# Kernel tuning notes

Hardware: AMD Instinct MI355X
Metric: run time of the kernel (lower is better)

The kernel has to match this reference:

```python
import jax, jax.numpy as jnp
import numpy as np


def setup_inputs() -> dict:
    key = jax.random.key(0)
    k1, _ = jax.random.split(key)
    x = jax.random.normal(k1, (8, 128, 56, 56), dtype=jnp.float32)
    gamma = jnp.array(0.5, dtype=jnp.float32)  # learned scalar (init gamma=0.5)
    return {"x": x, "gamma": gamma}


def reference(x, gamma):
    # conv=False path: query/key/value convs are Identity, so Q=K=V=x flattened.
    B, C, H, W = x.shape
    N = H * W
    v = x.reshape(B, C, N)                          # [B, C, N]
    # energy[b, i, j] = sum_c x[b, c, i] * x[b, c, j]  (Q^T K)
    energy = jnp.einsum('bci,bcj->bij', v, v)       # [B, N, N]
    # multiplicative mask: zero out the diagonal BEFORE softmax (not -inf)
    mask = 1.0 - jnp.eye(N, dtype=energy.dtype)
    attention = jax.nn.softmax(energy * mask, axis=-1)  # [B, N, N]
    # out = bmm(V, attention): out[b, c, j] = sum_i v[b, c, i] * attention[b, i, j]
    out = jnp.einsum('bci,bij->bcj', v, attention)  # [B, C, N]
    out = jax.nn.relu(out).reshape(B, C, H, W)
    y = gamma * out + x
    return (y, out, x, gamma)
```

## Files before the change

kernel.cpp:

```cpp
#include <hip/hip_runtime.h>
#include <math.h>

#define Bb 8
#define Cc 128
#define Nn 3136
#define Np 3200
#define Mm (Bb*Cc*Nn)
#define PADX 136
#define PADV 72
#define SHIFT 44.0f

typedef unsigned short u16;
typedef unsigned int   u32;
typedef __attribute__((ext_vector_type(8)))  u16      u16x8;
typedef __attribute__((ext_vector_type(8)))  _Float16 f16x8;
typedef __attribute__((ext_vector_type(4)))  _Float16 f16x4;
typedef __attribute__((ext_vector_type(4)))  float    f32x4;
typedef __attribute__((ext_vector_type(16))) float    f32x16;

__global__ __launch_bounds__(256) void prep_kernel(const float* __restrict__ x,
                                                   const float* __restrict__ gamma_p,
                                                   float* __restrict__ out,
                                                   u16* __restrict__ xt,
                                                   u16* __restrict__ xc,
                                                   float* __restrict__ row_d) {
    const int bx = blockIdx.x;
    const int b = bx / 50, nblk = bx % 50;
    const int t = threadIdx.x;

    if (nblk == 49) {
        const u16x8 z8 = {0, 0, 0, 0, 0, 0, 0, 0};
        #pragma unroll
        for (int it = 0; it < 4; ++it) {
            const int idx = it * 256 + t, row = idx / 17, seg = idx % 17;
            *(u16x8*)&xt[(size_t)(b * Np + Nn + row) * PADX + seg * 8] = z8;
        }
        if (t < 64) {
            const int idx = 1024 + t, row = idx / 17, seg = idx % 17;
            *(u16x8*)&xt[(size_t)(b * Np + Nn + row) * PADX + seg * 8] = z8;
        }
        #pragma unroll
        for (int it = 0; it < 4; ++it) {
            const int idx = it * 256 + t, c = idx >> 3, seg = idx & 7;
            *(u16x8*)&xc[(size_t)(b * Cc + c) * Np + Nn + seg * 8] = z8;
        }
        if (t < 64) row_d[b * Np + Nn + t] = 1.0f;
        return;
    }

    __shared__ float lx[Cc][65];
    const int n0 = nblk * 64;

    #pragma unroll 8
    for (int r = 0; r < 32; ++r) {
        const int c = r * 4 + (t >> 6);
        const int g = (b * Cc + c) * Nn + n0 + (t & 63);
        const float v = x[g];
        lx[c][t & 63] = v;
        out[(size_t)2 * Mm + g] = v;
    }
    __syncthreads();

    {
        const int nl = t & 63, cseg = t >> 6;
        u16x8 hv[4];
        #pragma unroll
        for (int cc = 0; cc < 32; ++cc) {
            const _Float16 hh = (_Float16)lx[cseg * 32 + cc][nl];
            hv[cc >> 3][cc & 7] = __builtin_bit_cast(u16, hh);
        }
        const size_t base = (size_t)(b * Np + n0 + nl) * PADX + cseg * 32;
        #pragma unroll
        for (int k = 0; k < 4; ++k) *(u16x8*)&xt[base + k * 8] = hv[k];
    }
    {
        const int c = t >> 1, half = t & 1;
        u16x8 hv[4];
        #pragma unroll
        for (int k = 0; k < 32; ++k) {
            const _Float16 hh = (_Float16)lx[c][half * 32 + k];
            hv[k >> 3][k & 7] = __builtin_bit_cast(u16, hh);
        }
        const size_t base = (size_t)(b * Cc + c) * Np + n0 + half * 32;
        #pragma unroll
        for (int k = 0; k < 4; ++k) *(u16x8*)&xc[base + k * 8] = hv[k];
    }
    if (bx == 0 && t == 0) out[(size_t)3 * Mm] = gamma_p[0];
}

__global__ __launch_bounds__(256, 3) void stats_kernel(const u16* __restrict__ xt,
                                                       float* __restrict__ row_d) {
    __shared__ u16 s_jt[64 * PADX];

    const int bx = blockIdx.x;
    const int b = bx / 196, rem = bx % 196;
    const int i0 = (rem >> 2) * 64, jq = rem & 3;
    const int t = threadIdx.x;
    const int w = t >> 6, l = t & 63, lane = l & 31, h = l >> 5;
    const int igrp = w & 1, jsub = w >> 1;

    f16x8 Bf[8];
    {
        const size_t rb = (size_t)(b * Np + i0 + igrp * 32 + lane) * PADX + h * 8;
        #pragma unroll
        for (int kk = 0; kk < 8; ++kk)
            Bf[kk] = *(const f16x8*)&xt[rb + kk * 16];
    }

    float sa = 0.0f, sb = 0.0f;
    const int jt0 = jq * 12 + (jq < 2 ? jq : 2);
    const int jcnt = 12 + (jq < 2 ? 1 : 0);

    for (int jt = jt0; jt < jt0 + jcnt; ++jt) {
        const int j0 = jt * 64;
        __syncthreads();
        {
            const u16* src = xt + (size_t)(b * Np + j0) * PADX;
            u16x8 tv[4], tv4;
            #pragma unroll
            for (int it = 0; it < 4; ++it)
                tv[it] = *(const u16x8*)&src[(it * 256 + t) * 8];
            if (t < 64) tv4 = *(const u16x8*)&src[(1024 + t) * 8];
            #pragma unroll
            for (int it = 0; it < 4; ++it)
                *(u16x8*)&s_jt[(it * 256 + t) * 8] = tv[it];
            if (t < 64) *(u16x8*)&s_jt[(1024 + t) * 8] = tv4;
        }
        __syncthreads();

        f32x16 ea, eb;
        #pragma unroll
        for (int r = 0; r < 16; ++r) { ea[r] = 0.0f; eb[r] = 0.0f; }
        const int arow = (jsub * 32 + lane) * PADX + h * 8;
        #pragma unroll
        for (int kk = 0; kk < 4; ++kk) {
            const f16x8 A0 = *(const f16x8*)&s_jt[arow + (2 * kk) * 16];
            const f16x8 A1 = *(const f16x8*)&s_jt[arow + (2 * kk + 1) * 16];
            ea = __builtin_amdgcn_mfma_f32_32x32x16_f16(A0, Bf[2 * kk], ea, 0, 0, 0);
            eb = __builtin_amdgcn_mfma_f32_32x32x16_f16(A1, Bf[2 * kk + 1], eb, 0, 0, 0);
        }

        const bool diag = (j0 == i0) && (jsub == igrp);
        #pragma unroll
        for (int r = 0; r < 16; ++r) {
            const int mrow = (r & 3) + 8 * (r >> 2) + 4 * h;
            float v = ea[r] + eb[r];
            if (diag && (mrow == lane)) v = 0.0f;
            if (r & 1) sb += __expf(v - SHIFT); else sa += __expf(v - SHIFT);
        }
    }

    float ssum = sa + sb;
    ssum += __shfl_xor(ssum, 32, 64);
    if (h == 0) atomicAdd(&row_d[b * Np + i0 + igrp * 32 + lane], ssum);
}

__global__ __launch_bounds__(256, 3) void out_kernel(const u16* __restrict__ xt,
                                                     const u16* __restrict__ xc,
                                                     const float* __restrict__ row_d,
                                                     float* __restrict__ out) {
    __shared__ u16 s_xt[64 * PADX];
    __shared__ u16 s_xc[Cc * PADV];
    __shared__ u16 s_pt[64 * PADV];

    const int bx = blockIdx.x;
    const int b = bx / 98, rem = bx % 98;
    const int j0 = (rem >> 1) * 64, ih = rem & 1;
    const int t = threadIdx.x;
    const int w = t >> 6, l = t & 63, lane = l & 31, h = l >> 5;
    const int isub = w & 1, jgrp = w >> 1;
    const int jg = w & 1,  cp = w >> 1;
    const u16* __restrict__ xtb = xt + (size_t)b * Np * PADX;
    const u16* __restrict__ xcb = xc + (size_t)b * Cc * Np;

    f16x8 Bj[8];
    {
        const size_t rb = (size_t)(j0 + jgrp * 32 + lane) * PADX + h * 8;
        #pragma unroll
        for (int kk = 0; kk < 8; ++kk)
            Bj[kk] = *(const f16x8*)&xtb[rb + kk * 16];
    }

    f32x16 oa, ob;
    #pragma unroll
    for (int r = 0; r < 16; ++r) { oa[r] = 0.0f; ob[r] = 0.0f; }

    for (int ti = ih * 25; ti < ih * 25 + 25; ++ti) {
        const int i0g = ti * 64;
        __syncthreads();
        {
            const u16* srct = xtb + (size_t)i0g * PADX;
            u16x8 vt[4], vt4, vcr[4];
            #pragma unroll
            for (int it = 0; it < 4; ++it) {
                vt[it] = *(const u16x8*)&srct[(it * 256 + t) * 8];
                const int q = it * 256 + t;
                vcr[it] = *(const u16x8*)&xcb[(size_t)(q >> 3) * Np + i0g + (q & 7) * 8];
            }
            if (t < 64) vt4 = *(const u16x8*)&srct[(1024 + t) * 8];
            #pragma unroll
            for (int it = 0; it < 4; ++it) {
                *(u16x8*)&s_xt[(it * 256 + t) * 8] = vt[it];
                const int q = it * 256 + t;
                *(u16x8*)&s_xc[(q >> 3) * PADV + (q & 7) * 8] = vcr[it];
            }
            if (t < 64) *(u16x8*)&s_xt[(1024 + t) * 8] = vt4;
        }
        __syncthreads();

        f32x16 ea, eb;
        #pragma unroll
        for (int r = 0; r < 16; ++r) { ea[r] = 0.0f; eb[r] = 0.0f; }
        const int arow = (isub * 32 + lane) * PADX + h * 8;
        #pragma unroll
        for (int kk = 0; kk < 4; ++kk) {
            const f16x8 A0 = *(const f16x8*)&s_xt[arow + (2 * kk) * 16];
            const f16x8 A1 = *(const f16x8*)&s_xt[arow + (2 * kk + 1) * 16];
            ea = __builtin_amdgcn_mfma_f32_32x32x16_f16(A0, Bj[2 * kk], ea, 0, 0, 0);
            eb = __builtin_amdgcn_mfma_f32_32x32x16_f16(A1, Bj[2 * kk + 1], eb, 0, 0, 0);
        }

        const bool mayDiag = (j0 < i0g + 64) && (i0g < j0 + 64);
        const int ptbase = (jgrp * 32 + lane) * PADV + isub * 32;
        #pragma unroll
        for (int q = 0; q < 4; ++q) {
            const f32x4 dq = *(const f32x4*)&row_d[b * Np + i0g + isub * 32 + q * 8 + h * 4];
            f16x4 pv;
            #pragma unroll
            for (int r = 0; r < 4; ++r) {
                const int m = q * 8 + h * 4 + r;
                float v = ea[q * 4 + r] + eb[q * 4 + r];
                if (mayDiag && (i0g + isub * 32 + m == j0 + jgrp * 32 + lane)) v = 0.0f;
                pv[r] = (_Float16)(__expf(v - SHIFT) * __builtin_amdgcn_rcpf(dq[r]));
            }
            *(f16x4*)&s_pt[ptbase + q * 8 + h * 4] = pv;
        }
        __syncthreads();

        const int pbrow = (jg * 32 + lane) * PADV + h * 8;
        const int va0 = (cp * 64 + lane) * PADV + h * 8;
        const int va1 = va0 + 32 * PADV;
        #pragma unroll
        for (int kk = 0; kk < 4; ++kk) {
            const f16x8 Bp  = *(const f16x8*)&s_pt[pbrow + kk * 16];
            const f16x8 Av0 = *(const f16x8*)&s_xc[va0 + kk * 16];
            const f16x8 Av1 = *(const f16x8*)&s_xc[va1 + kk * 16];
            oa = __builtin_amdgcn_mfma_f32_32x32x16_f16(Av0, Bp, oa, 0, 0, 0);
            ob = __builtin_amdgcn_mfma_f32_32x32x16_f16(Av1, Bp, ob, 0, 0, 0);
        }
    }

    #pragma unroll
    for (int r = 0; r < 16; ++r) {
        const int mrow = (r & 3) + 8 * (r >> 2) + 4 * h;
        const int jj = j0 + jg * 32 + lane;
        {
            const int c = cp * 64 + mrow;
            const size_t pos = (size_t)(b * Cc + c) * Nn + jj;
            out[(size_t)ih * Mm + pos] = oa[r];
        }
        {
            const int c = cp * 64 + 32 + mrow;
            const size_t pos = (size_t)(b * Cc + c) * Nn + jj;
            out[(size_t)ih * Mm + pos] = ob[r];
        }
    }
}

__global__ __launch_bounds__(256) void finish_kernel(const float* __restrict__ x,
                                                     const float* __restrict__ gamma_p,
                                                     float* __restrict__ out) {
    const float gamma = gamma_p[0];
    const size_t base = ((size_t)blockIdx.x * 256 + threadIdx.x) * 4;
    const f32x4 pa = *(const f32x4*)&out[base];
    const f32x4 pb = *(const f32x4*)&out[(size_t)Mm + base];
    const f32x4 xv = *(const f32x4*)&x[base];
    f32x4 yo, oo;
    #pragma unroll
    for (int r = 0; r < 4; ++r) {
        const float o = fmaxf(pa[r] + pb[r], 0.0f);
        oo[r] = o;
        yo[r] = fmaf(gamma, o, xv[r]);
    }
    *(f32x4*)&out[base] = yo;
    *(f32x4*)&out[(size_t)Mm + base] = oo;
}

extern "C" void kernel_launch(void* const* d_in, const int* in_sizes, int n_in,
                              void* d_out, int out_size, void* d_ws, size_t ws_size,
                              hipStream_t stream) {
    const float* x       = (const float*)d_in[0];
    const float* gamma_p = (const float*)d_in[1];
    float* out = (float*)d_out;

    float* row_d = (float*)d_ws;
    u16* xt = (u16*)((char*)d_ws + (1 << 17));
    u16* xc = xt + (size_t)Bb * Np * PADX;

    hipMemsetAsync(row_d, 0, (size_t)Bb * Np * sizeof(float), stream);
    prep_kernel  <<<400, 256, 0, stream>>>(x, gamma_p, out, xt, xc, row_d);
    stats_kernel <<<1568, 256, 0, stream>>>(xt, row_d);
    out_kernel   <<<784, 256, 0, stream>>>(xt, xc, row_d, out);
    finish_kernel<<<3136, 256, 0, stream>>>(x, gamma_p, out);
}
```

Before: 215.2 us.

## Store fp16 operands in MFMA-fragment tiled layout and read directly from global

Changes the fp16 copies of x into a tiled layout that matches the MFMA fragment layout, so stats and out kernels load A/V operands straight from global memory (L2) instead of staging through LDS with barriers. The P tile is double-buffered in shared memory, leaving one barrier per iteration. Softmax normalization is folded into a per-row log2 offset computed by a new small conv kernel, which replaces exp and reciprocal with a single exp2 of an fma. Diagonal masking gets a separate branch, stats occupancy is raised, and block index ordering interleaves batches. This adds a kernel launch and relies on L2/L1 serving repeated global loads efficiently.

```diff
diff --git a/kernel.cpp b/kernel.cpp
--- a/kernel.cpp
+++ b/kernel.cpp
@@ -5,24 +5,35 @@
 #define Cc 128
 #define Nn 3136
 #define Np 3200
+#define NT 50
 #define Mm (Bb*Cc*Nn)
-#define PADX 136
 #define PADV 72
-#define SHIFT 44.0f
+#define L2E 1.44269504088896340736f
+#define C44 (44.0f * L2E)
+
+#define XT2B (NT*16*64*8)
+#define XC2B (NT*8*128*8)
 
 typedef unsigned short u16;
-typedef unsigned int   u32;
 typedef __attribute__((ext_vector_type(8)))  u16      u16x8;
 typedef __attribute__((ext_vector_type(8)))  _Float16 f16x8;
 typedef __attribute__((ext_vector_type(4)))  _Float16 f16x4;
 typedef __attribute__((ext_vector_type(4)))  float    f32x4;
 typedef __attribute__((ext_vector_type(16))) float    f32x16;
 
+__device__ __forceinline__ float exp2fast(float x) {
+#if __has_builtin(__builtin_amdgcn_exp2f)
+    return __builtin_amdgcn_exp2f(x);
+#else
+    float r; asm volatile("v_exp_f32 %0, %1" : "=v"(r) : "v"(x)); return r;
+#endif
+}
+
 __global__ __launch_bounds__(256) void prep_kernel(const float* __restrict__ x,
                                                    const float* __restrict__ gamma_p,
                                                    float* __restrict__ out,
-                                                   u16* __restrict__ xt,
-                                                   u16* __restrict__ xc,
+                                                   u16* __restrict__ xt2,
+                                                   u16* __restrict__ xc2,
                                                    float* __restrict__ row_d) {
     const int bx = blockIdx.x;
     const int b = bx / 50, nblk = bx % 50;
@@ -30,19 +41,12 @@
 
     if (nblk == 49) {
         const u16x8 z8 = {0, 0, 0, 0, 0, 0, 0, 0};
+        u16* dt = xt2 + ((size_t)b * NT + 49) * (16 * 64 * 8);
+        u16* dc = xc2 + ((size_t)b * NT + 49) * (8 * 128 * 8);
         #pragma unroll
         for (int it = 0; it < 4; ++it) {
-            const int idx = it * 256 + t, row = idx / 17, seg = idx % 17;
-            *(u16x8*)&xt[(size_t)(b * Np + Nn + row) * PADX + seg * 8] = z8;
-        }
-        if (t < 64) {
-            const int idx = 1024 + t, row = idx / 17, seg = idx % 17;
-            *(u16x8*)&xt[(size_t)(b * Np + Nn + row) * PADX + seg * 8] = z8;
-        }
-        #pragma unroll
-        for (int it = 0; it < 4; ++it) {
-            const int idx = it * 256 + t, c = idx >> 3, seg = idx & 7;
-            *(u16x8*)&xc[(size_t)(b * Cc + c) * Np + Nn + seg * 8] = z8;
+            *(u16x8*)&dt[(it * 256 + t) * 8] = z8;
+            *(u16x8*)&dc[(it * 256 + t) * 8] = z8;
         }
         if (t < 64) row_d[b * Np + Nn + t] = 1.0f;
         return;
@@ -69,9 +73,9 @@
             const _Float16 hh = (_Float16)lx[cseg * 32 + cc][nl];
             hv[cc >> 3][cc & 7] = __builtin_bit_cast(u16, hh);
         }
-        const size_t base = (size_t)(b * Np + n0 + nl) * PADX + cseg * 32;
-        #pragma unroll
-        for (int k = 0; k < 4; ++k) *(u16x8*)&xt[base + k * 8] = hv[k];
+        u16* base = xt2 + (((size_t)(b * NT + nblk) * 16 + cseg * 4) * 64 + nl) * 8;
+        #pragma unroll
+        for (int k = 0; k < 4; ++k) *(u16x8*)&base[k * (64 * 8)] = hv[k];
     }
     {
         const int c = t >> 1, half = t & 1;
@@ -81,170 +85,149 @@
             const _Float16 hh = (_Float16)lx[c][half * 32 + k];
             hv[k >> 3][k & 7] = __builtin_bit_cast(u16, hh);
         }
-        const size_t base = (size_t)(b * Cc + c) * Np + n0 + half * 32;
-        #pragma unroll
-        for (int k = 0; k < 4; ++k) *(u16x8*)&xc[base + k * 8] = hv[k];
+        u16* base = xc2 + (((size_t)(b * NT + nblk) * 8 + half * 4) * 128 + c) * 8;
+        #pragma unroll
+        for (int k = 0; k < 4; ++k) *(u16x8*)&base[k * (128 * 8)] = hv[k];
     }
     if (bx == 0 && t == 0) out[(size_t)3 * Mm] = gamma_p[0];
 }
 
-__global__ __launch_bounds__(256, 3) void stats_kernel(const u16* __restrict__ xt,
+__global__ __launch_bounds__(256, 5) void stats_kernel(const u16* __restrict__ xt2,
                                                        float* __restrict__ row_d) {
-    __shared__ u16 s_jt[64 * PADX];
-
     const int bx = blockIdx.x;
-    const int b = bx / 196, rem = bx % 196;
-    const int i0 = (rem >> 2) * 64, jq = rem & 3;
+    const int b = bx & 7, rem = bx >> 3;
+    const int i0t = rem >> 2, jq = rem & 3;
     const int t = threadIdx.x;
     const int w = t >> 6, l = t & 63, lane = l & 31, h = l >> 5;
     const int igrp = w & 1, jsub = w >> 1;
+    const u16* __restrict__ xb = xt2 + (size_t)b * XT2B;
 
     f16x8 Bf[8];
-    {
-        const size_t rb = (size_t)(b * Np + i0 + igrp * 32 + lane) * PADX + h * 8;
-        #pragma unroll
-        for (int kk = 0; kk < 8; ++kk)
-            Bf[kk] = *(const f16x8*)&xt[rb + kk * 16];
-    }
-
-    float sa = 0.0f, sb = 0.0f;
+    const int irow = igrp * 32 + lane;
+    #pragma unroll
+    for (int kk = 0; kk < 8; ++kk)
+        Bf[kk] = *(const f16x8*)&xb[(((size_t)i0t * 16 + 2 * kk + h) * 64 + irow) * 8];
+
+    float sa = 0.f, sb = 0.f;
     const int jt0 = jq * 12 + (jq < 2 ? jq : 2);
     const int jcnt = 12 + (jq < 2 ? 1 : 0);
+    const int jrow = jsub * 32 + lane;
 
     for (int jt = jt0; jt < jt0 + jcnt; ++jt) {
-        const int j0 = jt * 64;
-        __syncthreads();
-        {
-            const u16* src = xt + (size_t)(b * Np + j0) * PADX;
-            u16x8 tv[4], tv4;
-            #pragma unroll
-            for (int it = 0; it < 4; ++it)
-                tv[it] = *(const u16x8*)&src[(it * 256 + t) * 8];
-            if (t < 64) tv4 = *(const u16x8*)&src[(1024 + t) * 8];
-            #pragma unroll
-            for (int it = 0; it < 4; ++it)
-                *(u16x8*)&s_jt[(it * 256 + t) * 8] = tv[it];
-            if (t < 64) *(u16x8*)&s_jt[(1024 + t) * 8] = tv4;
-        }
-        __syncthreads();
-
-        f32x16 ea, eb;
-        #pragma unroll
-        for (int r = 0; r < 16; ++r) { ea[r] = 0.0f; eb[r] = 0.0f; }
-        const int arow = (jsub * 32 + lane) * PADX + h * 8;
-        #pragma unroll
-        for (int kk = 0; kk < 4; ++kk) {
-            const f16x8 A0 = *(const f16x8*)&s_jt[arow + (2 * kk) * 16];
-            const f16x8 A1 = *(const f16x8*)&s_jt[arow + (2 * kk + 1) * 16];
-            ea = __builtin_amdgcn_mfma_f32_32x32x16_f16(A0, Bf[2 * kk], ea, 0, 0, 0);
-            eb = __builtin_amdgcn_mfma_f32_32x32x16_f16(A1, Bf[2 * kk + 1], eb, 0, 0, 0);
-        }
-
-        const bool diag = (j0 == i0) && (jsub == igrp);
-        #pragma unroll
-        for (int r = 0; r < 16; ++r) {
-            const int mrow = (r & 3) + 8 * (r >> 2) + 4 * h;
-            float v = ea[r] + eb[r];
-            if (diag && (mrow == lane)) v = 0.0f;
-            if (r & 1) sb += __expf(v - SHIFT); else sa += __expf(v - SHIFT);
-        }
-    }
-
+        const u16* ab = &xb[((size_t)jt * 16 * 64 + jrow) * 8];
+        f32x16 acc;
+        #pragma unroll
+        for (int r = 0; r < 16; ++r) acc[r] = 0.f;
+        #pragma unroll
+        for (int kk = 0; kk < 8; ++kk) {
+            const f16x8 A = *(const f16x8*)&ab[(2 * kk + h) * 512];
+            acc = __builtin_amdgcn_mfma_f32_32x32x16_f16(A, Bf[kk], acc, 0, 0, 0);
+        }
+        if (jt == i0t) {
+            const bool dsub = (jsub == igrp);
+            #pragma unroll
+            for (int r = 0; r < 16; ++r) {
+                const int mrow = (r & 3) + 8 * (r >> 2) + 4 * h;
+                float v = acc[r];
+                if (dsub && mrow == lane) v = 0.f;
+                const float e = exp2fast(fmaf(v, L2E, -C44));
+                if (r & 1) sb += e; else sa += e;
+            }
+        } else {
+            #pragma unroll
+            for (int r = 0; r < 16; ++r) {
+                const float e = exp2fast(fmaf(acc[r], L2E, -C44));
+                if (r & 1) sb += e; else sa += e;
+            }
+        }
+    }
     float ssum = sa + sb;
     ssum += __shfl_xor(ssum, 32, 64);
-    if (h == 0) atomicAdd(&row_d[b * Np + i0 + igrp * 32 + lane], ssum);
-}
-
-__global__ __launch_bounds__(256, 3) void out_kernel(const u16* __restrict__ xt,
-                                                     const u16* __restrict__ xc,
-                                                     const float* __restrict__ row_d,
+    if (h == 0) atomicAdd(&row_d[b * Np + i0t * 64 + igrp * 32 + lane], ssum);
+}
+
+__global__ __launch_bounds__(256) void conv_kernel(float* __restrict__ row_d) {
+    const int i = blockIdx.x * 256 + threadIdx.x;
+    row_d[i] = C44 + __log2f(row_d[i]);
+}
+
+__global__ __launch_bounds__(256, 3) void out_kernel(const u16* __restrict__ xt2,
+                                                     const u16* __restrict__ xc2,
+                                                     const float* __restrict__ row_c,
                                                      float* __restrict__ out) {
-    __shared__ u16 s_xt[64 * PADX];
-    __shared__ u16 s_xc[Cc * PADV];
-    __shared__ u16 s_pt[64 * PADV];
+    __shared__ u16 s_pt[2][64 * PADV];
 
     const int bx = blockIdx.x;
-    const int b = bx / 98, rem = bx % 98;
-    const int j0 = (rem >> 1) * 64, ih = rem & 1;
+    const int b = bx & 7, rem = bx >> 3;
+    const int j0t = rem >> 1, ih = rem & 1;
     const int t = threadIdx.x;
     const int w = t >> 6, l = t & 63, lane = l & 31, h = l >> 5;
     const int isub = w & 1, jgrp = w >> 1;
     const int jg = w & 1,  cp = w >> 1;
-    const u16* __restrict__ xtb = xt + (size_t)b * Np * PADX;
-    const u16* __restrict__ xcb = xc + (size_t)b * Cc * Np;
+    const u16* __restrict__ xtb = xt2 + (size_t)b * XT2B;
+    const u16* __restrict__ xcb = xc2 + (size_t)b * XC2B;
 
     f16x8 Bj[8];
-    {
-        const size_t rb = (size_t)(j0 + jgrp * 32 + lane) * PADX + h * 8;
-        #pragma unroll
-        for (int kk = 0; kk < 8; ++kk)
-            Bj[kk] = *(const f16x8*)&xtb[rb + kk * 16];
-    }
+    const int jrow = jgrp * 32 + lane;
+    #pragma unroll
+    for (int kk = 0; kk < 8; ++kk)
+        Bj[kk] = *(const f16x8*)&xtb[(((size_t)j0t * 16 + 2 * kk + h) * 64 + jrow) * 8];
 
     f32x16 oa, ob;
     #pragma unroll
-    for (int r = 0; r < 16; ++r) { oa[r] = 0.0f; ob[r] = 0.0f; }
+    for (int r = 0; r < 16; ++r) { oa[r] = 0.f; ob[r] = 0.f; }
+
+    const int arow = isub * 32 + lane;
+    const int ptbase = (jgrp * 32 + lane) * PADV + isub * 32;
+    const int pbrow = (jg * 32 + lane) * PADV + h * 8;
 
     for (int ti = ih * 25; ti < ih * 25 + 25; ++ti) {
-        const int i0g = ti * 64;
+        f32x16 ea;
+        #pragma unroll
+        for (int r = 0; r < 16; ++r) ea[r] = 0.f;
+        const u16* ab = &xtb[((size_t)ti * 16 * 64 + arow) * 8];
+        #pragma unroll
+        for (int kk = 0; kk < 8; ++kk) {
+            const f16x8 A = *(const f16x8*)&ab[(2 * kk + h) * 512];
+            ea = __builtin_amdgcn_mfma_f32_32x32x16_f16(A, Bj[kk], ea, 0, 0, 0);
+        }
+
+        u16* pt = &s_pt[ti & 1][0];
+        const float* cbase = &row_c[b * Np + ti * 64 + isub * 32];
+        if (ti == j0t) {
+            const bool dsub = (isub == jgrp);
+            #pragma unroll
+            for (int q = 0; q < 4; ++q) {
+                const f32x4 cv = *(const f32x4*)&cbase[q * 8 + h * 4];
+                f16x4 pv;
+                #pragma unroll
+                for (int r = 0; r < 4; ++r) {
+                    const int m = q * 8 + h * 4 + r;
+                    float v = ea[q * 4 + r];
+                    if (dsub && m == lane) v = 0.f;
+                    pv[r] = (_Float16)exp2fast(fmaf(v, L2E, -cv[r]));
+                }
+                *(f16x4*)&pt[ptbase + q * 8 + h * 4] = pv;
+            }
+        } else {
+            #pragma unroll
+            for (int q = 0; q < 4; ++q) {
+                const f32x4 cv = *(const f32x4*)&cbase[q * 8 + h * 4];
+                f16x4 pv;
+                #pragma unroll
+                for (int r = 0; r < 4; ++r)
+                    pv[r] = (_Float16)exp2fast(fmaf(ea[q * 4 + r], L2E, -cv[r]));
+                *(f16x4*)&pt[ptbase + q * 8 + h * 4] = pv;
+            }
+        }
         __syncthreads();
-        {
-            const u16* srct = xtb + (size_t)i0g * PADX;
-            u16x8 vt[4], vt4, vcr[4];
-            #pragma unroll
-            for (int it = 0; it < 4; ++it) {
-                vt[it] = *(const u16x8*)&srct[(it * 256 + t) * 8];
-                const int q = it * 256 + t;
-                vcr[it] = *(const u16x8*)&xcb[(size_t)(q >> 3) * Np + i0g + (q & 7) * 8];
-            }
-            if (t < 64) vt4 = *(const u16x8*)&srct[(1024 + t) * 8];
-            #pragma unroll
-            for (int it = 0; it < 4; ++it) {
-                *(u16x8*)&s_xt[(it * 256 + t) * 8] = vt[it];
-                const int q = it * 256 + t;
-                *(u16x8*)&s_xc[(q >> 3) * PADV + (q & 7) * 8] = vcr[it];
-            }
-            if (t < 64) *(u16x8*)&s_xt[(1024 + t) * 8] = vt4;
-        }
-        __syncthreads();
-
-        f32x16 ea, eb;
-        #pragma unroll
-        for (int r = 0; r < 16; ++r) { ea[r] = 0.0f; eb[r] = 0.0f; }
-        const int arow = (isub * 32 + lane) * PADX + h * 8;
+
+        const u16* vb = &xcb[((size_t)ti * 8 * 128 + cp * 64 + lane) * 8];
         #pragma unroll
         for (int kk = 0; kk < 4; ++kk) {
-            const f16x8 A0 = *(const f16x8*)&s_xt[arow + (2 * kk) * 16];
-            const f16x8 A1 = *(const f16x8*)&s_xt[arow + (2 * kk + 1) * 16];
-            ea = __builtin_amdgcn_mfma_f32_32x32x16_f16(A0, Bj[2 * kk], ea, 0, 0, 0);
-            eb = __builtin_amdgcn_mfma_f32_32x32x16_f16(A1, Bj[2 * kk + 1], eb, 0, 0, 0);
-        }
-
-        const bool mayDiag = (j0 < i0g + 64) && (i0g < j0 + 64);
-        const int ptbase = (jgrp * 32 + lane) * PADV + isub * 32;
-        #pragma unroll
-        for (int q = 0; q < 4; ++q) {
-            const f32x4 dq = *(const f32x4*)&row_d[b * Np + i0g + isub * 32 + q * 8 + h * 4];
-            f16x4 pv;
-            #pragma unroll
-            for (int r = 0; r < 4; ++r) {
-                const int m = q * 8 + h * 4 + r;
-                float v = ea[q * 4 + r] + eb[q * 4 + r];
-                if (mayDiag && (i0g + isub * 32 + m == j0 + jgrp * 32 + lane)) v = 0.0f;
-                pv[r] = (_Float16)(__expf(v - SHIFT) * __builtin_amdgcn_rcpf(dq[r]));
-            }
-            *(f16x4*)&s_pt[ptbase + q * 8 + h * 4] = pv;
-        }
-        __syncthreads();
-
-        const int pbrow = (jg * 32 + lane) * PADV + h * 8;
-        const int va0 = (cp * 64 + lane) * PADV + h * 8;
-        const int va1 = va0 + 32 * PADV;
-        #pragma unroll
-        for (int kk = 0; kk < 4; ++kk) {
-            const f16x8 Bp  = *(const f16x8*)&s_pt[pbrow + kk * 16];
-            const f16x8 Av0 = *(const f16x8*)&s_xc[va0 + kk * 16];
-            const f16x8 Av1 = *(const f16x8*)&s_xc[va1 + kk * 16];
+            const f16x8 Bp  = *(const f16x8*)&pt[pbrow + kk * 16];
+            const f16x8 Av0 = *(const f16x8*)&vb[((2 * kk + h) * 128) * 8];
+            const f16x8 Av1 = *(const f16x8*)&vb[((2 * kk + h) * 128 + 32) * 8];
             oa = __builtin_amdgcn_mfma_f32_32x32x16_f16(Av0, Bp, oa, 0, 0, 0);
             ob = __builtin_amdgcn_mfma_f32_32x32x16_f16(Av1, Bp, ob, 0, 0, 0);
         }
@@ -253,7 +236,7 @@
     #pragma unroll
     for (int r = 0; r < 16; ++r) {
         const int mrow = (r & 3) + 8 * (r >> 2) + 4 * h;
-        const int jj = j0 + jg * 32 + lane;
+        const int jj = j0t * 64 + jg * 32 + lane;
         {
             const int c = cp * 64 + mrow;
             const size_t pos = (size_t)(b * Cc + c) * Nn + jj;
@@ -294,12 +277,13 @@
     float* out = (float*)d_out;
 
     float* row_d = (float*)d_ws;
-    u16* xt = (u16*)((char*)d_ws + (1 << 17));
-    u16* xc = xt + (size_t)Bb * Np * PADX;
+    u16* xt2 = (u16*)((char*)d_ws + (1 << 17));
+    u16* xc2 = xt2 + (size_t)Bb * XT2B;
 
     hipMemsetAsync(row_d, 0, (size_t)Bb * Np * sizeof(float), stream);
-    prep_kernel  <<<400, 256, 0, stream>>>(x, gamma_p, out, xt, xc, row_d);
-    stats_kernel <<<1568, 256, 0, stream>>>(xt, row_d);
-    out_kernel   <<<784, 256, 0, stream>>>(xt, xc, row_d, out);
+    prep_kernel  <<<400, 256, 0, stream>>>(x, gamma_p, out, xt2, xc2, row_d);
+    stats_kernel <<<1568, 256, 0, stream>>>(xt2, row_d);
+    conv_kernel  <<<100, 256, 0, stream>>>(row_d);
+    out_kernel   <<<784, 256, 0, stream>>>(xt2, xc2, row_d, out);
     finish_kernel<<<3136, 256, 0, stream>>>(x, gamma_p, out);
 }
```

New measurement: 190.9 us. 1.13x faster.
